# Kernel optimization log

Measured on AMD Instinct MI355X. Metric: run time of the kernel, lower is better.

Reference implementation:

```python
import jax, jax.numpy as jnp
import numpy as np

EMBED_DIMS = 128
NUM_HEADS = 4
NUM_LAYERS = 3
OUT_CHANNELS = 20
PROJECT_SCALE = 4
VOXEL_SIZE = 0.2
SCENE_FULL = (256, 256, 32)
SCENE = tuple(s // PROJECT_SCALE for s in SCENE_FULL)  # (64, 64, 8)
NQ = SCENE[0] * SCENE[1] * SCENE[2]                    # 32768
N_INST = 100
NUM_CLS = 21
IMAGE_SHAPE = (48, 160)
ORI_IMAGE_SHAPE = (384, 1280)
SCORE_THR, MASK_THR, IOU_THR = 0.25, 0.5, 0.8
DILATIONS = (1, 2, 3)


def _generate_grid(grid_shape, value):
    axes = [np.linspace(0, v - 1, s, dtype=np.float32) for s, v in zip(grid_shape, value)]
    return np.stack(np.meshgrid(*axes, indexing='ij'), 0)


def _layer_norm(x, g, b):
    mu = x.mean(-1, keepdims=True)
    var = ((x - mu) ** 2).mean(-1, keepdims=True)
    return (x - mu) * jax.lax.rsqrt(var + 1e-5) * g + b


def _mha(q, k, v, bias, in_w, in_b, out_w, out_b):
    C = q.shape[-1]
    H, D = NUM_HEADS, q.shape[-1] // NUM_HEADS
    wq, wk, wv = jnp.split(in_w, 3, axis=0)
    bq, bk, bv = jnp.split(in_b, 3)
    qh = (q @ wq.T + bq).reshape(q.shape[0], q.shape[1], H, D)
    kh = (k @ wk.T + bk).reshape(k.shape[0], k.shape[1], H, D)
    vh = (v @ wv.T + bv).reshape(v.shape[0], v.shape[1], H, D)
    s = jnp.einsum('bqhd,bkhd->bhqk', qh, kh) * (1.0 / np.sqrt(D)) + bias
    a = jax.nn.softmax(s, axis=-1)
    o = jnp.einsum('bhqk,bkhd->bqhd', a, vh).reshape(q.shape)
    return o @ out_w.T + out_b


def _conv3d(x, w, b, dilation):
    pad = (w.shape[-1] // 2) * dilation
    y = jax.lax.conv_general_dilated(
        x, w, window_strides=(1, 1, 1), padding=[(pad, pad)] * 3,
        rhs_dilation=(dilation,) * 3,
        dimension_numbers=('NCDHW', 'OIDHW', 'NCDHW'))
    return y + b[None, :, None, None, None]


def _forward(inst_queries, pred_logits, pred_masks, depth, K, E, voxel_origin,
             query_embed_w, pos_embed_w, attn_in_w, attn_in_b, attn_out_w,
             attn_out_b, ln1_g, ln1_b, ffn_w1, ffn_b1, ffn_w2, ffn_b2,
             ln2_g, ln2_b, proc_w, proc_b, out_w, out_b, fov_mask):
    C = EMBED_DIMS
    h, w = IMAGE_SHAPE
    n = pred_masks.shape[1]
    # buffers (compile-time constants)
    image_grid = jnp.asarray(_generate_grid(IMAGE_SHAPE, ORI_IMAGE_SHAPE)[::-1].copy())  # [2,h,w] (x,y)
    qp = (_generate_grid(SCENE, SCENE) + 0.5) * VOXEL_SIZE * PROJECT_SCALE
    query_pos0 = jnp.asarray(qp.reshape(3, -1).T)[None]  # [1,NQ,3]

    # panoptic postprocess (masked form, bs=1; invalid instance slots masked, not dropped)
    probs = jax.nn.softmax(jax.nn.sigmoid(pred_logits) / 0.06, axis=-1)
    scores = probs.max(-1)[0]              # [n]; labels.ne(num_classes) always True
    keep0 = scores > SCORE_THR
    pm = jax.nn.sigmoid(pred_masks[0])     # [n,h,w]
    prob_masks = jnp.where(keep0[:, None, None], scores[:, None, None] * pm, -1.0)
    mask_ids = jnp.argmax(prob_masks, axis=0)   # [h,w]
    masks = (mask_ids[None] == jnp.arange(n)[:, None, None]) & keep0[:, None, None]
    mask_area = masks.reshape(n, -1).sum(-1).astype(jnp.float32)
    pm_bin = pm >= MASK_THR
    pm_area = pm_bin.reshape(n, -1).sum(-1).astype(jnp.float32)
    masks = masks & pm_bin
    inter = masks.reshape(n, -1).sum(-1)
    keep = keep0 & (inter > 0) & (mask_area >= IOU_THR * pm_area)
    masks = masks & keep[:, None, None]
    any_keep = keep.any()

    # gather_mask_pos: back-project masked pixels to 3D and sum per instance
    d = depth.reshape(1, 1, h, w)
    grid = jnp.concatenate([image_grid[None] * d, d], axis=1).reshape(1, 3, h * w)
    cam = jnp.linalg.inv(K) @ grid
    hom = jnp.concatenate([cam, jnp.ones((1, 1, h * w), cam.dtype)], axis=1)
    pts = (jnp.linalg.inv(E) @ hom)[0, :3].T       # [HW,3]
    inst_xyz = masks.reshape(n, -1).astype(pts.dtype) @ pts  # [n,3] gather-mask-sum
    inst_pos = (inst_xyz @ pos_embed_w.T)[None]    # [1,n,C]

    # cross-attention over all scene queries; fov gather/scatter folded into final where,
    # valid because per-query computation is independent in cross-attn + per-token FFN/LN.
    qpos = (query_pos0 + voxel_origin) @ pos_embed_w.T        # [1,NQ,C]
    use = jnp.where(any_keep, 1.0, 0.0).astype(inst_queries.dtype)
    kv_k = inst_queries + use * inst_pos
    key_mask = jnp.where(any_keep, keep, True)
    bias = jnp.where(key_mask, 0.0, -1e9)[None, None, None, :]  # [1,1,1,n]
    q = query_embed_w[None]
    for li in range(NUM_LAYERS):
        x = q + qpos
        a = _mha(x, kv_k, inst_queries, bias, attn_in_w[li], attn_in_b[li],
                 attn_out_w[li], attn_out_b[li])
        x = _layer_norm(a + x, ln1_g[li], ln1_b[li])
        f = jax.nn.gelu(x @ ffn_w1[li].T + ffn_b1[li], approximate=False) @ ffn_w2[li].T + ffn_b2[li]
        q = _layer_norm(f + x, ln2_g[li], ln2_b[li])

    q = jnp.where(fov_mask[..., None], q, query_embed_w[None])   # scatter-update query_embed_src[fov_mask]
    x3d = q.reshape(1, *SCENE, C).transpose(0, 4, 1, 2, 3)       # [1,C,X,Y,Z]
    for i, dil in enumerate(DILATIONS):                          # Process: dilated residual convs
        x3d = jax.nn.relu(_conv3d(x3d, proc_w[i], proc_b[i], dil) + x3d)
    return _conv3d(x3d, out_w, out_b, 1)                         # [1,out_ch,X,Y,Z]


def setup_inputs():
    key = jax.random.key(0)
    ks = jax.random.split(key, 16)
    C, L = EMBED_DIMS, NUM_LAYERS
    s = 0.02
    inp = {}
    inp['inst_queries'] = jax.random.normal(ks[0], (1, N_INST, C), jnp.float32)
    inp['pred_logits'] = jax.random.normal(ks[1], (1, N_INST, NUM_CLS), jnp.float32)
    inp['pred_masks'] = jax.random.normal(ks[2], (1, N_INST) + IMAGE_SHAPE, jnp.float32) * 2.0
    inp['depth'] = jax.random.uniform(ks[3], (1,) + IMAGE_SHAPE, jnp.float32, 1.0, 50.0)
    inp['K'] = jnp.array([[[500.0, 0.0, 640.0], [0.0, 500.0, 192.0], [0.0, 0.0, 1.0]]], jnp.float32)
    inp['E'] = jnp.eye(4, dtype=jnp.float32).at[:3, 3].set(jnp.array([0.5, -0.3, 1.2]))[None]
    inp['voxel_origin'] = jax.random.normal(ks[4], (1, 1, 3), jnp.float32)
    inp['query_embed_w'] = jax.random.normal(ks[5], (NQ, C), jnp.float32) * s
    inp['pos_embed_w'] = jax.random.normal(ks[6], (C, 3), jnp.float32) * 2e-4
    inp['attn_in_w'] = jax.random.normal(ks[7], (L, 3 * C, C), jnp.float32) * s
    inp['attn_in_b'] = jnp.zeros((L, 3 * C), jnp.float32)
    inp['attn_out_w'] = jax.random.normal(ks[8], (L, C, C), jnp.float32) * s
    inp['attn_out_b'] = jnp.zeros((L, C), jnp.float32)
    inp['ln1_g'] = jnp.ones((L, C), jnp.float32)
    inp['ln1_b'] = jnp.zeros((L, C), jnp.float32)
    inp['ffn_w1'] = jax.random.normal(ks[9], (L, 4 * C, C), jnp.float32) * s
    inp['ffn_b1'] = jnp.zeros((L, 4 * C), jnp.float32)
    inp['ffn_w2'] = jax.random.normal(ks[10], (L, C, 4 * C), jnp.float32) * s
    inp['ffn_b2'] = jnp.zeros((L, C), jnp.float32)
    inp['ln2_g'] = jnp.ones((L, C), jnp.float32)
    inp['ln2_b'] = jnp.zeros((L, C), jnp.float32)
    inp['proc_w'] = jax.random.normal(ks[11], (3, C, C, 3, 3, 3), jnp.float32) * s
    inp['proc_b'] = jnp.zeros((3, C), jnp.float32)
    inp['out_w'] = jax.random.normal(ks[12], (OUT_CHANNELS, C, 1, 1, 1), jnp.float32) * s
    inp['out_b'] = jnp.zeros((OUT_CHANNELS,), jnp.float32)
    inp['fov_mask'] = jax.random.bernoulli(ks[13], 0.5, (1, NQ))
    return inp


def reference(inst_queries, pred_logits, pred_masks, depth, K, E, voxel_origin,
              query_embed_w, pos_embed_w, attn_in_w, attn_in_b, attn_out_w,
              attn_out_b, ln1_g, ln1_b, ffn_w1, ffn_b1, ffn_w2, ffn_b2,
              ln2_g, ln2_b, proc_w, proc_b, out_w, out_b, fov_mask):
    return _forward(inst_queries, pred_logits, pred_masks, depth, K, E, voxel_origin,
                    query_embed_w, pos_embed_w, attn_in_w, attn_in_b, attn_out_w,
                    attn_out_b, ln1_g, ln1_b, ffn_w1, ffn_b1, ffn_w2, ffn_b2,
                    ln2_g, ln2_b, proc_w, proc_b, out_w, out_b, fov_mask)
```

## Files before the change

kernel.cpp:

```cpp
#include <hip/hip_runtime.h>
#include <math.h>

typedef unsigned short u16;
typedef unsigned int   u32;

#define NQv 32768
#define HWp 7680
#define NI  100

typedef short v8s __attribute__((ext_vector_type(8)));
typedef float v4f __attribute__((ext_vector_type(4)));

__device__ inline float bf2f(u16 u){ u32 x = ((u32)u) << 16; return __uint_as_float(x); }
__device__ inline u16 f2bf(float f){
  u32 x = __float_as_uint(f);
  u32 r = (x + 0x7fffu + ((x >> 16) & 1u)) >> 16;
  return (u16)r;
}
__device__ inline float sigf(float x){ return 1.0f / (1.0f + expf(-x)); }

typedef const __attribute__((address_space(1))) void* gas_t;
typedef __attribute__((address_space(3))) void* las_t;

__global__ void k_prep_small(const float* __restrict__ Km, const float* __restrict__ Em,
                             const float* __restrict__ logits,
                             float* __restrict__ mats, float* __restrict__ scores,
                             int* __restrict__ keep0)
{
  int tid = threadIdx.x;
  if (tid == 0) {
    double a[9];
    for (int i = 0; i < 9; i++) a[i] = (double)Km[i];
    double det = a[0]*(a[4]*a[8]-a[5]*a[7]) - a[1]*(a[3]*a[8]-a[5]*a[6]) + a[2]*(a[3]*a[7]-a[4]*a[6]);
    double id = 1.0 / det;
    double inv[9];
    inv[0]=(a[4]*a[8]-a[5]*a[7])*id; inv[1]=(a[2]*a[7]-a[1]*a[8])*id; inv[2]=(a[1]*a[5]-a[2]*a[4])*id;
    inv[3]=(a[5]*a[6]-a[3]*a[8])*id; inv[4]=(a[0]*a[8]-a[2]*a[6])*id; inv[5]=(a[2]*a[3]-a[0]*a[5])*id;
    inv[6]=(a[3]*a[7]-a[4]*a[6])*id; inv[7]=(a[1]*a[6]-a[0]*a[7])*id; inv[8]=(a[0]*a[4]-a[1]*a[3])*id;
    for (int i = 0; i < 9; i++) mats[i] = (float)inv[i];
    double m[4][8];
    for (int r = 0; r < 4; r++){
      for (int c = 0; c < 4; c++){ m[r][c] = (double)Em[r*4+c]; m[r][4+c] = (r==c) ? 1.0 : 0.0; }
    }
    for (int col = 0; col < 4; col++){
      int piv = col; double best = fabs(m[col][col]);
      for (int r = col+1; r < 4; r++){ double v = fabs(m[r][col]); if (v > best){ best = v; piv = r; } }
      if (piv != col){ for (int c = 0; c < 8; c++){ double t = m[col][c]; m[col][c] = m[piv][c]; m[piv][c] = t; } }
      double p = m[col][col];
      for (int c = 0; c < 8; c++) m[col][c] /= p;
      for (int r = 0; r < 4; r++) if (r != col){ double f = m[r][col]; for (int c = 0; c < 8; c++) m[r][c] -= f*m[col][c]; }
    }
    for (int r = 0; r < 3; r++) for (int c = 0; c < 4; c++) mats[9 + r*4 + c] = (float)m[r][4+c];
  }
  if (tid < NI) {
    float mx = -1e30f;
    for (int c = 0; c < 21; c++){ float t = sigf(logits[tid*21+c]) / 0.06f; mx = fmaxf(mx, t); }
    float s = 0.f;
    for (int c = 0; c < 21; c++){ float t = sigf(logits[tid*21+c]) / 0.06f; s += expf(t - mx); }
    float sc = 1.0f / s;
    scores[tid] = sc;
    keep0[tid] = (sc > 0.25f) ? 1 : 0;
  }
}

__global__ void k_prep_multi(
    const float* __restrict__ s0, u16* __restrict__ d0, int n0,
    const float* __restrict__ s1, u16* __restrict__ d1, int n1,
    const float* __restrict__ s2, u16* __restrict__ d2, int n2,
    const float* __restrict__ s3, u16* __restrict__ d3, int n3,
    u16* __restrict__ z0, int zn0, u16* __restrict__ z1, int zn1,
    u16* __restrict__ z2, int zn2,
    const float* __restrict__ pe, float* __restrict__ peT)
{
  int i = blockIdx.x*256 + threadIdx.x;
  if (i < n0){ d0[i] = f2bf(s0[i]); return; } i -= n0;
  if (i < n1){ d1[i] = f2bf(s1[i]); return; } i -= n1;
  if (i < n2){ d2[i] = f2bf(s2[i]); return; } i -= n2;
  if (i < n3){ d3[i] = f2bf(s3[i]); return; } i -= n3;
  if (i < zn0){ z0[i] = 0; return; } i -= zn0;
  if (i < zn1){ z1[i] = 0; return; } i -= zn1;
  if (i < zn2){ z2[i] = 0; return; } i -= zn2;
  if (i < 384){ int d = i >> 7, c = i & 127; peT[i] = pe[c*3 + d]; }
}

__global__ __launch_bounds__(256) void k_mask_argmax2(
    const float* __restrict__ pmL, const float* __restrict__ scores,
    const int* __restrict__ keep0, int* __restrict__ mids)
{
  __shared__ float sv[4][64];
  __shared__ int   si[4][64];
  int tid = threadIdx.x, lane = tid & 63, w = tid >> 6;
  int p = blockIdx.x*64 + lane;
  float best = -2e30f; int bid = 0;
  #pragma unroll 5
  for (int jj = 0; jj < 25; jj++){
    int i = w*25 + jj;
    float lg = pmL[i*HWp + p];
    float val = keep0[i] ? scores[i] * sigf(lg) : -1.0f;
    if (val > best){ best = val; bid = i; }
  }
  sv[w][lane] = best; si[w][lane] = bid;
  __syncthreads();
  if (w == 0){
    float b0 = sv[0][lane]; int i0 = si[0][lane];
    #pragma unroll
    for (int g = 1; g < 4; g++){
      float bg = sv[g][lane]; int ig = si[g][lane];
      if (bg > b0 || (bg == b0 && ig < i0)){ b0 = bg; i0 = ig; }
    }
    mids[p] = i0;
  }
}

__global__ __launch_bounds__(256) void k_instbp(
    const float* __restrict__ pmL, const int* __restrict__ mids,
    const int* __restrict__ keep0, const float* __restrict__ depth,
    const float* __restrict__ mats, int* __restrict__ keep, float* __restrict__ xyz)
{
  int i = blockIdx.x, tid = threadIdx.x;
  int k0 = keep0[i];
  int ma = 0, pa = 0, it = 0;
  for (int p = tid; p < HWp; p += 256){
    float lg = pmL[i*HWp + p];
    int pb = (lg >= 0.0f) ? 1 : 0;
    int mi = (mids[p] == i && k0) ? 1 : 0;
    ma += mi; pa += pb; it += (mi & pb);
  }
  __shared__ int sma[256], spa[256], sit[256];
  __shared__ int s_keep;
  sma[tid] = ma; spa[tid] = pa; sit[tid] = it;
  __syncthreads();
  for (int off = 128; off; off >>= 1){
    if (tid < off){ sma[tid]+=sma[tid+off]; spa[tid]+=spa[tid+off]; sit[tid]+=sit[tid+off]; }
    __syncthreads();
  }
  if (tid == 0){
    int kk = (k0 && sit[0] > 0 && ((float)sma[0] >= 0.8f*(float)spa[0])) ? 1 : 0;
    keep[i] = kk; s_keep = kk;
  }
  __syncthreads();
  float sx = 0.f, sy = 0.f, sz = 0.f;
  if (s_keep){
    float ik0=mats[0],ik1=mats[1],ik2=mats[2],ik3=mats[3],ik4=mats[4],ik5=mats[5],ik6=mats[6],ik7=mats[7],ik8=mats[8];
    const float* iE = mats + 9;
    for (int p = tid; p < HWp; p += 256){
      if (mids[p] == i && pmL[i*HWp + p] >= 0.0f){
        int r = p / 160, c = p % 160;
        float xg = (float)((double)c * (1279.0/159.0));
        float yg = (float)((double)r * (383.0/47.0));
        float d = depth[p];
        float g0 = xg*d, g1 = yg*d, g2 = d;
        float c0 = ik0*g0 + ik1*g1 + ik2*g2;
        float c1 = ik3*g0 + ik4*g1 + ik5*g2;
        float c2 = ik6*g0 + ik7*g1 + ik8*g2;
        sx += iE[0]*c0 + iE[1]*c1 + iE[2]*c2 + iE[3];
        sy += iE[4]*c0 + iE[5]*c1 + iE[6]*c2 + iE[7];
        sz += iE[8]*c0 + iE[9]*c1 + iE[10]*c2 + iE[11];
      }
    }
  }
  __shared__ float rx[256], ry[256], rz[256];
  rx[tid]=sx; ry[tid]=sy; rz[tid]=sz;
  __syncthreads();
  for (int off = 128; off; off >>= 1){
    if (tid < off){ rx[tid]+=rx[tid+off]; ry[tid]+=ry[tid+off]; rz[tid]+=rz[tid+off]; }
    __syncthreads();
  }
  if (tid == 0){ xyz[i*3+0]=rx[0]; xyz[i*3+1]=ry[0]; xyz[i*3+2]=rz[0]; }
}

__global__ void k_kvk(const float* __restrict__ iq, const float* __restrict__ pe,
                      const float* __restrict__ xyz, const int* __restrict__ keep,
                      float* __restrict__ kvk)
{
  int tid = threadIdx.x;
  unsigned long long b = __ballot(tid < 100 && keep[tid] != 0);
  __shared__ int s_w[4];
  if ((tid & 63) == 0) s_w[tid >> 6] = (b != 0ULL);
  __syncthreads();
  float u = (s_w[0] | s_w[1]) ? 1.0f : 0.0f;
  int idx = blockIdx.x*256 + tid;
  if (idx >= NI*128) return;
  int i = idx >> 7, c = idx & 127;
  float ip = pe[c*3+0]*xyz[i*3+0] + pe[c*3+1]*xyz[i*3+1] + pe[c*3+2]*xyz[i*3+2];
  kvk[idx] = iq[idx] + u * ip;
}

__global__ __launch_bounds__(512) void k_khvh2(const float* __restrict__ kvk,
    const float* __restrict__ iq, const float* __restrict__ Win,
    const float* __restrict__ bin, const int* __restrict__ keep,
    float* __restrict__ biasArr, u16* __restrict__ khs_bf, u16* __restrict__ vt_bf)
{
  __shared__ u16 s_in[NI][130];
  __shared__ u16 s_w[64][130];
  __shared__ int s_any[8];
  int li = blockIdx.x, c0 = blockIdx.y*64;
  bool isK = (c0 < 128);
  const float* srcIn = isK ? kvk : iq;
  int tid = threadIdx.x;
  unsigned long long bm = __ballot(tid < 100 && keep[tid] != 0);
  if ((tid & 63) == 0) s_any[tid >> 6] = (bm != 0ULL);
  for (int i = tid; i < NI*128; i += 512) s_in[i>>7][i&127] = f2bf(srcIn[i]);
  const float* wbase = Win + ((size_t)li*384 + 128 + c0)*128;
  for (int i = tid; i < 64*128; i += 512) s_w[i>>7][i&127] = f2bf(wbase[i]);
  __syncthreads();
  if (li == 0 && c0 == 0 && tid < 128){
    int any = s_any[0] | s_any[1];
    float bb;
    if (tid < NI) bb = any ? (keep[tid] ? 0.0f : -1e9f) : 0.0f;
    else bb = -1e9f;
    biasArr[tid] = bb;
  }
  for (int o = tid; o < NI*64; o += 512){
    int k = o >> 6, c = o & 63;
    float acc = 0.f;
    #pragma unroll 8
    for (int j = 0; j < 128; j++) acc += bf2f(s_in[k][j]) * bf2f(s_w[c][j]);
    int cc = c0 + c;
    float v = acc + bin[li*384 + 128 + cc];
    int ch = cc & 127;
    if (isK) khs_bf[(((size_t)li*4 + (ch>>5))*128 + k)*32 + (ch&31)] = f2bf(v * 0.17677669529663687f);
    else     vt_bf [(((size_t)li*4 + (ch>>5))*32 + (ch&31))*128 + k] = f2bf(v);
  }
}

__global__ __launch_bounds__(256) void k_packconv2(const float* __restrict__ w, u16* __restrict__ wp)
{
  __shared__ u16 s[3456];
  int o = blockIdx.x, li = blockIdx.y;
  const float* src = w + ((size_t)li*128 + o)*3456;
  for (int t = threadIdx.x; t < 3456; t += 256) s[t] = f2bf(src[t]);
  __syncthreads();
  for (int e = threadIdx.x; e < 3456; e += 256){
    int t = e >> 7, i = e & 127;
    wp[(((size_t)li*27 + t)*128 + o)*128 + i] = s[i*27 + t];
  }
}

__device__ inline void stage128(const u16* __restrict__ G, u16* lds,
                                int rbase, int pitchK, int kofs)
{
  int lane = threadIdx.x & 63, w = threadIdx.x >> 6;
  #pragma unroll
  for (int s = 0; s < 4; s++){
    int ldsOff = s*8192 + w*1024 + lane*16;
    int row = ldsOff >> 8;
    int cb  = ldsOff & 255;
    int scb = cb ^ ((row & 7) << 4);
    const u16* src = G + (size_t)(rbase + row)*pitchK + kofs + (scb >> 1);
    u16* dst = lds + (s*4096 + w*512);
    __builtin_amdgcn_global_load_lds((gas_t)src, (las_t)dst, 16, 0, 0);
  }
}

__device__ inline void copy32k(const u16* __restrict__ G, u16* lds)
{
  int lane = threadIdx.x & 63, w = threadIdx.x >> 6;
  #pragma unroll
  for (int s = 0; s < 4; s++){
    int off = s*4096 + w*512;
    const u16* src = G + off + lane*8;
    __builtin_amdgcn_global_load_lds((gas_t)src, (las_t)(lds + off), 16, 0, 0);
  }
}

__device__ inline void stageConvA4(const u16* __restrict__ X, const u16* __restrict__ zp,
                                   u16* lds, int m0, int dx, int dy)
{
  int lane = threadIdx.x & 63, w = threadIdx.x >> 6;
  #pragma unroll
  for (int s = 0; s < 4; s++){
    int ldsOff = s*8192 + w*1024 + lane*16;
    int row = ldsOff >> 8;
    int cb  = ldsOff & 255;
    int scb = cb ^ ((row & 7) << 4);
    int sidx = m0 + row;
    int xs = (sidx >> 9) + dx, ys = ((sidx >> 3) & 63) + dy, zs = sidx & 7;
    bool ok = ((unsigned)xs < 64u) & ((unsigned)ys < 64u);
    const u16* src = ok ? (X + (size_t)((xs*64+ys)*8+zs)*128 + (scb>>1)) : (zp + (scb>>1));
    u16* dst = lds + (s*4096 + w*512);
    __builtin_amdgcn_global_load_lds((gas_t)src, (las_t)dst, 16, 0, 0);
  }
}

__device__ inline v8s fragld(const u16* base, int row, int cb){
  return *(const v8s*)(base + row*128 + (((cb) ^ ((row & 7) << 4)) >> 1));
}

__device__ inline void compute128(const u16* As, const u16* Bs,
                                  int wm, int wn, int r15, int kg, v4f acc[2][4])
{
  #pragma unroll
  for (int k0 = 0; k0 < 4; k0++){
    int cb = k0*64 + kg*16;
    v8s a0 = fragld(As, wm*32 +      r15, cb);
    v8s a1 = fragld(As, wm*32 + 16 + r15, cb);
    v8s b0 = fragld(Bs, wn*64 +      r15, cb);
    v8s b1 = fragld(Bs, wn*64 + 16 + r15, cb);
    v8s b2 = fragld(Bs, wn*64 + 32 + r15, cb);
    v8s b3 = fragld(Bs, wn*64 + 48 + r15, cb);
    acc[0][0] = __builtin_amdgcn_mfma_f32_16x16x32_bf16(a0, b0, acc[0][0], 0, 0, 0);
    acc[0][1] = __builtin_amdgcn_mfma_f32_16x16x32_bf16(a0, b1, acc[0][1], 0, 0, 0);
    acc[0][2] = __builtin_amdgcn_mfma_f32_16x16x32_bf16(a0, b2, acc[0][2], 0, 0, 0);
    acc[0][3] = __builtin_amdgcn_mfma_f32_16x16x32_bf16(a0, b3, acc[0][3], 0, 0, 0);
    acc[1][0] = __builtin_amdgcn_mfma_f32_16x16x32_bf16(a1, b0, acc[1][0], 0, 0, 0);
    acc[1][1] = __builtin_amdgcn_mfma_f32_16x16x32_bf16(a1, b1, acc[1][1], 0, 0, 0);
    acc[1][2] = __builtin_amdgcn_mfma_f32_16x16x32_bf16(a1, b2, acc[1][2], 0, 0, 0);
    acc[1][3] = __builtin_amdgcn_mfma_f32_16x16x32_bf16(a1, b3, acc[1][3], 0, 0, 0);
  }
}

__global__ __launch_bounds__(512) void k_layer(
    const void* __restrict__ srcv, int srcBf,
    const float* __restrict__ peT, const float* __restrict__ vo,
    const u16* __restrict__ ainQ, const float* __restrict__ ainQb,
    const u16* __restrict__ khs, const u16* __restrict__ vt,
    const float* __restrict__ biasArr,
    const u16* __restrict__ aoutw, const float* __restrict__ aoutb,
    const float* __restrict__ g1, const float* __restrict__ b1v,
    const u16* __restrict__ w1p, const float* __restrict__ b1p,
    const u16* __restrict__ w2p, const float* __restrict__ b2p,
    const float* __restrict__ g2, const float* __restrict__ b2v,
    u16* __restrict__ outB, const int* __restrict__ fov, const float* __restrict__ qe)
{
  extern __shared__ u16 smem[];
  u16* SA = smem;
  u16* SB = smem + 16384;
  u16* X  = smem + 32768;
  u16* Rh = smem + 49152;
  char* Xc = (char*)X;
  char* Rc = (char*)Rh;
  int tid = threadIdx.x, lane = tid & 63, w = tid >> 6;
  int wm = w & 3, wn = w >> 2, r15 = lane & 15, kg = lane >> 4;
  int m0 = blockIdx.x * 128;

  stage128(ainQ, SA, 0, 128, 0);
  copy32k(khs, Rh);
  copy32k(vt, Rh + 16384);
  {
    int r = tid >> 2, c0 = (tid & 3)*32;
    int q = m0 + r;
    float px = ((float)(q >> 9)       + 0.5f)*0.8f + vo[0];
    float py = ((float)((q >> 3)&63)  + 0.5f)*0.8f + vo[1];
    float pz = ((float)(q & 7)        + 0.5f)*0.8f + vo[2];
    char* arow = Xc + r*256;
    int rx = (r & 7) << 4;
    if (!srcBf){
      const float4* sp  = (const float4*)((const float*)srcv + (size_t)q*128 + c0);
      const float4* pex = (const float4*)(peT +   0 + c0);
      const float4* pey = (const float4*)(peT + 128 + c0);
      const float4* pez = (const float4*)(peT + 256 + c0);
      #pragma unroll
      for (int j = 0; j < 8; j++){
        float4 v = sp[j];
        float4 ax = pex[j], ay = pey[j], az = pez[j];
        float o0 = v.x + ax.x*px + ay.x*py + az.x*pz;
        float o1 = v.y + ax.y*px + ay.y*py + az.y*pz;
        float o2 = v.z + ax.z*px + ay.z*py + az.z*pz;
        float o3 = v.w + ax.w*px + ay.w*py + az.w*pz;
        int cbyte = (c0 + j*4)*2;
        *(u32*)(arow + ((cbyte    ) ^ rx)) = (u32)f2bf(o0) | ((u32)f2bf(o1) << 16);
        *(u32*)(arow + ((cbyte + 4) ^ rx)) = (u32)f2bf(o2) | ((u32)f2bf(o3) << 16);
      }
    } else {
      const u16* sp = (const u16*)srcv + (size_t)q*128 + c0;
      #pragma unroll
      for (int j = 0; j < 4; j++){
        v8s t = *(const v8s*)(sp + j*8);
        #pragma unroll
        for (int pr = 0; pr < 4; pr++){
          int c = c0 + j*8 + pr*2;
          float e0 = bf2f((u16)t[pr*2])   + peT[c]*px   + peT[128+c]*py   + peT[256+c]*pz;
          float e1 = bf2f((u16)t[pr*2+1]) + peT[c+1]*px + peT[128+c+1]*py + peT[256+c+1]*pz;
          *(u32*)(arow + ((c*2) ^ rx)) = (u32)f2bf(e0) | ((u32)f2bf(e1) << 16);
        }
      }
    }
  }
  __syncthreads();

  {
    v4f acc[2][4] = {};
    compute128(X, SA, wm, wn, r15, kg, acc);
    #pragma unroll
    for (int i = 0; i < 2; i++){
      #pragma unroll
      for (int j = 0; j < 4; j++){
        int col = wn*64 + j*16 + r15;
        float bv = ainQb[col];
        #pragma unroll
        for (int rr = 0; rr < 4; rr++){
          int row = wm*32 + i*16 + kg*4 + rr;
          *(u16*)((char*)SB + row*256 + (((col*2)) ^ ((row & 7) << 4))) = f2bf(acc[i][j][rr] + bv);
        }
      }
    }
  }
  __syncthreads();

  {
    int c = lane & 15, r4 = lane >> 4;
    char* pwc = (char*)(SA + w*2048);
    int qrow_base = w*16;
    #pragma unroll
    for (int h = 0; h < 4; h++){
      const u16* Kh = Rh + h*4096;
      const u16* Vh = Rh + 16384 + h*4096;
      int qrow = qrow_base + c;
      v8s qf = *(const v8s*)((char*)SB + qrow*256 + ((h*64 + r4*16) ^ ((qrow & 7) << 4)));
      v4f s[8] = {{0,0,0,0},{0,0,0,0},{0,0,0,0},{0,0,0,0},{0,0,0,0},{0,0,0,0},{0,0,0,0},{0,0,0,0}};
      #pragma unroll
      for (int kt = 0; kt < 8; kt++){
        v8s kf = *(const v8s*)(Kh + (kt*16 + c)*32 + r4*8);
        s[kt] = __builtin_amdgcn_mfma_f32_16x16x32_bf16(kf, qf, s[kt], 0, 0, 0);
      }
      float mx = -1e30f;
      #pragma unroll
      for (int kt = 0; kt < 8; kt++){
        float4 bb = *(const float4*)(biasArr + kt*16 + r4*4);
        s[kt][0] += bb.x; s[kt][1] += bb.y; s[kt][2] += bb.z; s[kt][3] += bb.w;
        mx = fmaxf(mx, fmaxf(fmaxf(s[kt][0], s[kt][1]), fmaxf(s[kt][2], s[kt][3])));
      }
      mx = fmaxf(mx, __shfl_xor(mx, 16, 64));
      mx = fmaxf(mx, __shfl_xor(mx, 32, 64));
      float sum = 0.f;
      #pragma unroll
      for (int kt = 0; kt < 8; kt++){
        #pragma unroll
        for (int rg = 0; rg < 4; rg++){
          float p = __expf(s[kt][rg] - mx);
          s[kt][rg] = p; sum += p;
        }
      }
      sum += __shfl_xor(sum, 16, 64);
      sum += __shfl_xor(sum, 32, 64);
      float inv = 1.0f / sum;
      int rxq = (c & 7) << 4;
      #pragma unroll
      for (int kt = 0; kt < 8; kt++){
        #pragma unroll
        for (int pr = 0; pr < 2; pr++){
          u32 pk = (u32)f2bf(s[kt][pr*2]*inv) | ((u32)f2bf(s[kt][pr*2+1]*inv) << 16);
          int colb = kt*32 + r4*8 + pr*4;
          *(u32*)(pwc + c*256 + (colb ^ rxq)) = pk;
        }
      }
      v4f o[2] = {{0,0,0,0},{0,0,0,0}};
      #pragma unroll
      for (int ks = 0; ks < 4; ks++){
        v8s aP = *(const v8s*)(pwc + c*256 + ((ks*64 + r4*16) ^ rxq));
        #pragma unroll
        for (int dt = 0; dt < 2; dt++){
          v8s vf = *(const v8s*)(Vh + (dt*16 + c)*128 + ks*32 + r4*8);
          o[dt] = __builtin_amdgcn_mfma_f32_16x16x32_bf16(aP, vf, o[dt], 0, 0, 0);
        }
      }
      #pragma unroll
      for (int dt = 0; dt < 2; dt++){
        #pragma unroll
        for (int rg = 0; rg < 4; rg++){
          int row = qrow_base + r4*4 + rg;
          int col = h*32 + dt*16 + c;
          *(u16*)((char*)SB + row*256 + ((col*2) ^ ((row & 7) << 4))) = f2bf(o[dt][rg]);
        }
      }
    }
  }
  __syncthreads();

  stage128(aoutw, SA, 0, 128, 0);
  __syncthreads();
  {
    v4f acc[2][4] = {};
    compute128(SB, SA, wm, wn, r15, kg, acc);
    #pragma unroll
    for (int i = 0; i < 2; i++){
      #pragma unroll
      for (int j = 0; j < 4; j++){
        int col = wn*64 + j*16 + r15;
        float bv = aoutb[col];
        #pragma unroll
        for (int rr = 0; rr < 4; rr++){
          int row = wm*32 + i*16 + kg*4 + rr;
          float xres = bf2f(*(const u16*)(Xc + row*256 + ((col*2) ^ ((row & 7) << 4))));
          float y = acc[i][j][rr] + bv + xres;
          *(float*)(Rc + row*512 + ((col*4) ^ ((row & 7) << 4))) = y;
        }
      }
    }
  }
  __syncthreads();

  {
    int r = tid >> 2, j4 = tid & 3;
    float vals[32];
    int rx = (r & 7) << 4;
    #pragma unroll
    for (int k = 0; k < 32; k++){
      int c = j4 + 4*k;
      vals[k] = *(const float*)(Rc + r*512 + ((c*4) ^ rx));
    }
    float s = 0.f;
    #pragma unroll
    for (int k = 0; k < 32; k++) s += vals[k];
    s += __shfl_xor(s, 1, 64); s += __shfl_xor(s, 2, 64);
    float mean = s * (1.0f/128.0f);
    float vv = 0.f;
    #pragma unroll
    for (int k = 0; k < 32; k++){ float d = vals[k] - mean; vv += d*d; }
    vv += __shfl_xor(vv, 1, 64); vv += __shfl_xor(vv, 2, 64);
    float rs = rsqrtf(vv*(1.0f/128.0f) + 1e-5f);
    #pragma unroll
    for (int k = 0; k < 32; k++){
      int c = j4 + 4*k;
      float o = (vals[k] - mean)*rs*g1[c] + b1v[c];
      *(float*)(Rc + r*512 + ((c*4) ^ rx)) = o;
      *(u16*)(Xc + r*256 + ((c*2) ^ rx)) = f2bf(o);
    }
  }
  __syncthreads();

  v4f acc2[2][4] = {};
  for (int nt = 0; nt < 4; nt++){
    stage128(w1p, SA, nt*128, 128, 0);
    stage128(w2p, SB, 0, 512, nt*128);
    __syncthreads();
    v4f a1[2][4] = {};
    compute128(X, SA, wm, wn, r15, kg, a1);
    __syncthreads();
    #pragma unroll
    for (int i = 0; i < 2; i++){
      #pragma unroll
      for (int j = 0; j < 4; j++){
        int col = wn*64 + j*16 + r15;
        float bv = b1p[nt*128 + col];
        #pragma unroll
        for (int rr = 0; rr < 4; rr++){
          int row = wm*32 + i*16 + kg*4 + rr;
          float hv = a1[i][j][rr] + bv;
          hv = 0.5f*hv*(1.0f + erff(hv*0.70710678118654752f));
          *(u16*)((char*)SA + row*256 + ((col*2) ^ ((row & 7) << 4))) = f2bf(hv);
        }
      }
    }
    __syncthreads();
    compute128(SA, SB, wm, wn, r15, kg, acc2);
    __syncthreads();
  }

  {
    #pragma unroll
    for (int i = 0; i < 2; i++){
      #pragma unroll
      for (int j = 0; j < 4; j++){
        int col = wn*64 + j*16 + r15;
        float bv = b2p[col];
        #pragma unroll
        for (int rr = 0; rr < 4; rr++){
          int row = wm*32 + i*16 + kg*4 + rr;
          char* p = Rc + row*512 + ((col*4) ^ ((row & 7) << 4));
          float y = acc2[i][j][rr] + bv + *(const float*)p;
          *(float*)p = y;
        }
      }
    }
  }
  __syncthreads();

  {
    int r = tid >> 2, j4 = tid & 3;
    float vals[32];
    int rx = (r & 7) << 4;
    #pragma unroll
    for (int k = 0; k < 32; k++){
      int c = j4 + 4*k;
      vals[k] = *(const float*)(Rc + r*512 + ((c*4) ^ rx));
    }
    float s = 0.f;
    #pragma unroll
    for (int k = 0; k < 32; k++) s += vals[k];
    s += __shfl_xor(s, 1, 64); s += __shfl_xor(s, 2, 64);
    float mean = s * (1.0f/128.0f);
    float vv = 0.f;
    #pragma unroll
    for (int k = 0; k < 32; k++){ float d = vals[k] - mean; vv += d*d; }
    vv += __shfl_xor(vv, 1, 64); vv += __shfl_xor(vv, 2, 64);
    float rs = rsqrtf(vv*(1.0f/128.0f) + 1e-5f);
    int gq = m0 + r;
    #pragma unroll
    for (int k = 0; k < 32; k++){
      int c = j4 + 4*k;
      float o = (vals[k] - mean)*rs*g2[c] + b2v[c];
      if (fov){
        outB[(size_t)gq*128 + c] = f2bf(fov[gq] ? o : qe[(size_t)gq*128 + c]);
      } else {
        outB[(size_t)gq*128 + c] = f2bf(o);
      }
    }
  }
}

__global__ __launch_bounds__(512) void k_conv4(
    const u16* __restrict__ X, const u16* __restrict__ W,
    const float* __restrict__ bias, const u16* __restrict__ zp,
    u16* __restrict__ Y, int dil)
{
  extern __shared__ u16 smem[];
  u16* bufA0 = smem;
  u16* bufA1 = smem + 16384;
  u16* bufW0 = smem + 32768;
  u16* bufW1 = smem + 49152;
  int tid = threadIdx.x, lane = tid & 63, w = tid >> 6;
  int wk = w & 1, wm = (w >> 1) & 1, wn = (w >> 2) & 1;
  int r15 = lane & 15, kg = lane >> 4;
  int bid = blockIdx.x;
  int lb = (bid & 7)*32 + (bid >> 3);
  int m0 = lb*128;
  v4f acc[4][4] = {};
  const v8s vzero = {0,0,0,0,0,0,0,0};
  stageConvA4(X, zp, bufA0, m0, -dil, -dil);
  stage128(W, bufW0, 0, 128, 0);
  for (int g = 0; g < 9; g++){
    const u16* As = (g & 1) ? bufA1 : bufA0;
    #pragma unroll
    for (int dzi = 0; dzi < 3; dzi++){
      int t = g*3 + dzi;
      const u16* Ws = (t & 1) ? bufW1 : bufW0;
      if (t + 1 < 27)
        stage128(W + (size_t)(t+1)*16384, ((t+1)&1) ? bufW1 : bufW0, 0, 128, 0);
      if (dzi == 0 && g < 8){
        int gn = g + 1;
        stageConvA4(X, zp, (gn & 1) ? bufA1 : bufA0, m0, (gn/3 - 1)*dil, (gn%3 - 1)*dil);
      }
      if (dzi == 0){
        if (g < 8) asm volatile("s_waitcnt vmcnt(8)" ::: "memory");
        else       asm volatile("s_waitcnt vmcnt(4)" ::: "memory");
      } else {
        if (t < 26) asm volatile("s_waitcnt vmcnt(4)" ::: "memory");
        else        asm volatile("s_waitcnt vmcnt(0)" ::: "memory");
      }
      __builtin_amdgcn_s_barrier();
      asm volatile("" ::: "memory");
      int zofs = (dzi - 1)*dil;
      bool okz = (unsigned)((r15 & 7) + zofs) < 8u;
      #pragma unroll
      for (int k0 = 0; k0 < 2; k0++){
        int cb = wk*128 + k0*64 + kg*16;
        v8s a[4], b[4];
        #pragma unroll
        for (int q = 0; q < 4; q++){
          int ra = wm*64 + q*16 + r15 + zofs;
          int rc = min(max(ra, 0), 127);
          a[q] = okz ? fragld(As, rc, cb) : vzero;
          b[q] = fragld(Ws, wn*64 + q*16 + r15, cb);
        }
        #pragma unroll
        for (int i = 0; i < 4; i++)
          #pragma unroll
          for (int j = 0; j < 4; j++)
            acc[i][j] = __builtin_amdgcn_mfma_f32_16x16x32_bf16(a[i], b[j], acc[i][j], 0, 0, 0);
      }
      asm volatile("" ::: "memory");
      __builtin_amdgcn_s_barrier();
      asm volatile("" ::: "memory");
    }
  }
  float* red = (float*)smem;
  if (wk == 0){
    #pragma unroll
    for (int i = 0; i < 4; i++)
      #pragma unroll
      for (int j = 0; j < 4; j++)
        #pragma unroll
        for (int rr = 0; rr < 4; rr++)
          red[(wm*64 + i*16 + kg*4 + rr)*128 + wn*64 + j*16 + r15] = acc[i][j][rr];
  }
  __syncthreads();
  if (wk == 1){
    #pragma unroll
    for (int i = 0; i < 4; i++){
      #pragma unroll
      for (int j = 0; j < 4; j++){
        int col = wn*64 + j*16 + r15;
        float bv = bias[col];
        #pragma unroll
        for (int rr = 0; rr < 4; rr++){
          int row = wm*64 + i*16 + kg*4 + rr;
          int grow = m0 + row;
          float v = acc[i][j][rr] + red[row*128 + col] + bv + bf2f(X[(size_t)grow*128 + col]);
          v = fmaxf(v, 0.0f);
          Y[(size_t)grow*128 + col] = f2bf(v);
        }
      }
    }
  }
}

__global__ __launch_bounds__(256) void k_outconv(const u16* __restrict__ X,
    const float* __restrict__ W, const float* __restrict__ B, float* __restrict__ out)
{
  __shared__ float sw[20*128];
  __shared__ float sbb[20];
  int tid = threadIdx.x;
  for (int i = tid; i < 20*128; i += 256) sw[i] = W[i];
  if (tid < 20) sbb[tid] = B[tid];
  __syncthreads();
  int s = blockIdx.x*256 + tid;
  u32 rv[64];
  const u32* xp = (const u32*)(X + (size_t)s*128);
  #pragma unroll
  for (int j = 0; j < 64; j++) rv[j] = xp[j];
  for (int ot = 0; ot < 20; ot++){
    float acc = sbb[ot];
    #pragma unroll
    for (int j = 0; j < 64; j++){
      u32 u = rv[j];
      acc += bf2f((u16)(u & 0xffff))*sw[ot*128 + 2*j] + bf2f((u16)(u >> 16))*sw[ot*128 + 2*j + 1];
    }
    out[(size_t)ot*NQv + s] = acc;
  }
}

extern "C" void kernel_launch(void* const* d_in, const int* in_sizes, int n_in,
                              void* d_out, int out_size, void* d_ws, size_t ws_size,
                              hipStream_t stream)
{
  const float* iq    = (const float*)d_in[0];
  const float* logits= (const float*)d_in[1];
  const float* pmL   = (const float*)d_in[2];
  const float* depth = (const float*)d_in[3];
  const float* Km    = (const float*)d_in[4];
  const float* Em    = (const float*)d_in[5];
  const float* vo    = (const float*)d_in[6];
  const float* qe    = (const float*)d_in[7];
  const float* pe    = (const float*)d_in[8];
  const float* ain_w = (const float*)d_in[9];
  const float* ain_b = (const float*)d_in[10];
  const float* aout_w= (const float*)d_in[11];
  const float* aout_b= (const float*)d_in[12];
  const float* ln1g  = (const float*)d_in[13];
  const float* ln1b  = (const float*)d_in[14];
  const float* w1    = (const float*)d_in[15];
  const float* b1    = (const float*)d_in[16];
  const float* w2    = (const float*)d_in[17];
  const float* b2    = (const float*)d_in[18];
  const float* ln2g  = (const float*)d_in[19];
  const float* ln2b  = (const float*)d_in[20];
  const float* pw    = (const float*)d_in[21];
  const float* pb    = (const float*)d_in[22];
  const float* ow    = (const float*)d_in[23];
  const float* ob    = (const float*)d_in[24];
  const int*   fov   = (const int*)d_in[25];
  float* out = (float*)d_out;

  (void)hipFuncSetAttribute((const void*)k_layer, hipFuncAttributeMaxDynamicSharedMemorySize, 163840);
  (void)hipFuncSetAttribute((const void*)k_conv4, hipFuncAttributeMaxDynamicSharedMemorySize, 131072);

  char* ws = (char*)d_ws;
  size_t off = 0;
  auto alloc = [&](size_t bytes) -> char* {
    char* p = ws + off;
    off = (off + bytes + 255) & ~(size_t)255;
    return p;
  };
  float* mats    = (float*)alloc(32*4);
  float* scores  = (float*)alloc(128*4);
  int*   keep0   = (int*)  alloc(128*4);
  int*   keep    = (int*)  alloc(128*4);
  float* biasArr = (float*)alloc(128*4);
  float* xyz     = (float*)alloc(512*4);
  u16*   zp      = (u16*)  alloc(256);
  float* peT     = (float*)alloc(384*4);
  int*   mids    = (int*)  alloc((size_t)HWp*4);
  float* kvkb    = (float*)alloc((size_t)NI*128*4);
  u16* khs_bf  = (u16*)alloc((size_t)3*4*128*32*2);
  u16* vt_bf   = (u16*)alloc((size_t)3*4*32*128*2);
  u16* ain_bf  = (u16*)alloc((size_t)3*384*128*2);
  u16* aout_bf = (u16*)alloc((size_t)3*128*128*2);
  u16* w1_bf   = (u16*)alloc((size_t)3*512*128*2);
  u16* w2_bf   = (u16*)alloc((size_t)3*128*512*2);
  u16* wc_bf   = (u16*)alloc((size_t)3*27*128*128*2);
  u16* T2bf = (u16*)alloc((size_t)NQv*128*2);
  u16* x3a  = (u16*)alloc((size_t)NQv*128*2);
  u16* x3b  = (u16*)alloc((size_t)NQv*128*2);
  (void)ws_size; (void)in_sizes; (void)n_in; (void)out_size;

  k_prep_small<<<1,128,0,stream>>>(Km, Em, logits, mats, scores, keep0);
  {
    int n0 = 3*384*128, n1 = 3*128*128, n2 = 3*512*128, n3 = 3*128*512;
    int zn0 = 3*4*128*32, zn1 = 3*4*32*128, zn2 = 128;
    int total = n0+n1+n2+n3+zn0+zn1+zn2+384;
    k_prep_multi<<<(total+255)/256,256,0,stream>>>(
        ain_w, ain_bf, n0, aout_w, aout_bf, n1, w1, w1_bf, n2, w2, w2_bf, n3,
        khs_bf, zn0, vt_bf, zn1, zp, zn2, pe, peT);
  }
  k_packconv2<<<dim3(128,3),256,0,stream>>>(pw, wc_bf);
  k_mask_argmax2<<<120,256,0,stream>>>(pmL, scores, keep0, mids);
  k_instbp<<<NI,256,0,stream>>>(pmL, mids, keep0, depth, mats, keep, xyz);
  k_kvk<<<(NI*128+255)/256,256,0,stream>>>(iq, pe, xyz, keep, kvkb);
  { dim3 g(3,4); k_khvh2<<<g,512,0,stream>>>(kvkb, iq, ain_w, ain_b, keep, biasArr, khs_bf, vt_bf); }

  for (int li = 0; li < 3; li++){
    const void* src = (li == 0) ? (const void*)qe : (const void*)T2bf;
    u16* outT = (li < 2) ? T2bf : x3a;
    k_layer<<<256,512,163840,stream>>>(
        src, (li == 0) ? 0 : 1, peT, vo,
        ain_bf + (size_t)li*384*128, ain_b + li*384,
        khs_bf + (size_t)li*16384, vt_bf + (size_t)li*16384, biasArr,
        aout_bf + (size_t)li*128*128, aout_b + li*128,
        ln1g + li*128, ln1b + li*128,
        w1_bf + (size_t)li*512*128, b1 + li*512,
        w2_bf + (size_t)li*128*512, b2 + li*128,
        ln2g + li*128, ln2b + li*128,
        outT, (li == 2) ? fov : nullptr, qe);
  }

  k_conv4<<<256,512,131072,stream>>>(x3a, wc_bf + (size_t)0*27*16384, pb + 0,   zp, x3b, 1);
  k_conv4<<<256,512,131072,stream>>>(x3b, wc_bf + (size_t)1*27*16384, pb + 128, zp, x3a, 2);
  k_conv4<<<256,512,131072,stream>>>(x3a, wc_bf + (size_t)2*27*16384, pb + 256, zp, x3b, 3);
  k_outconv<<<128,256,0,stream>>>(x3b, ow, ob, out);
}
```

Baseline: 361.4 us.

## Double-buffer FFN weight staging and use tanh-approx GELU

Restructures the FFN loop so the next chunk's W1/W2 tiles are staged into a second LDS buffer (reusing the fp32 residual region) while the current chunk computes, removing a barrier-bound serial load phase. The fp32 LayerNorm output is no longer kept in LDS; the second residual is read back from the bf16 copy, which lowers residual precision. The exact erf GELU is replaced with a tanh approximation built on __expf, which is cheaper but numerically slightly different.

```diff
diff --git a/kernel.cpp b/kernel.cpp
--- a/kernel.cpp
+++ b/kernel.cpp
@@ -491,6 +491,8 @@
   }
   __syncthreads();
 
+  stage128(w1p, SA, 0, 128, 0);
+  stage128(w2p, SB, 0, 512, 0);
   {
     int r = tid >> 2, j4 = tid & 3;
     float vals[32];
@@ -514,39 +516,53 @@
     for (int k = 0; k < 32; k++){
       int c = j4 + 4*k;
       float o = (vals[k] - mean)*rs*g1[c] + b1v[c];
-      *(float*)(Rc + r*512 + ((c*4) ^ rx)) = o;
       *(u16*)(Xc + r*256 + ((c*2) ^ rx)) = f2bf(o);
     }
   }
   __syncthreads();
 
   v4f acc2[2][4] = {};
-  for (int nt = 0; nt < 4; nt++){
-    stage128(w1p, SA, nt*128, 128, 0);
-    stage128(w2p, SB, 0, 512, nt*128);
-    __syncthreads();
-    v4f a1[2][4] = {};
-    compute128(X, SA, wm, wn, r15, kg, a1);
-    __syncthreads();
-    #pragma unroll
-    for (int i = 0; i < 2; i++){
-      #pragma unroll
-      for (int j = 0; j < 4; j++){
-        int col = wn*64 + j*16 + r15;
-        float bv = b1p[nt*128 + col];
-        #pragma unroll
-        for (int rr = 0; rr < 4; rr++){
-          int row = wm*32 + i*16 + kg*4 + rr;
-          float hv = a1[i][j][rr] + bv;
-          hv = 0.5f*hv*(1.0f + erff(hv*0.70710678118654752f));
-          *(u16*)((char*)SA + row*256 + ((col*2) ^ ((row & 7) << 4))) = f2bf(hv);
-        }
-      }
-    }
-    __syncthreads();
-    compute128(SA, SB, wm, wn, r15, kg, acc2);
-    __syncthreads();
-  }
+  {
+    u16* pa[2] = {SA, Rh};
+    u16* pb[2] = {SB, Rh + 16384};
+    for (int nt = 0; nt < 4; nt++){
+      u16* Wa = pa[nt & 1];
+      u16* Wb = pb[nt & 1];
+      if (nt > 0) __syncthreads();
+      if (nt < 3){
+        stage128(w1p, pa[(nt+1)&1], (nt+1)*128, 128, 0);
+        stage128(w2p, pb[(nt+1)&1], 0, 512, (nt+1)*128);
+      }
+      v4f a1[2][4] = {};
+      compute128(X, Wa, wm, wn, r15, kg, a1);
+      asm volatile("s_waitcnt lgkmcnt(0)" ::: "memory");
+      __builtin_amdgcn_s_barrier();
+      __builtin_amdgcn_sched_barrier(0);
+      #pragma unroll
+      for (int i = 0; i < 2; i++){
+        #pragma unroll
+        for (int j = 0; j < 4; j++){
+          int col = wn*64 + j*16 + r15;
+          float bv = b1p[nt*128 + col];
+          #pragma unroll
+          for (int rr = 0; rr < 4; rr++){
+            int row = wm*32 + i*16 + kg*4 + rr;
+            float hv = a1[i][j][rr] + bv;
+            float u2 = hv*(0.7978845608028654f + 0.0356774081f*hv*hv);
+            float e = __expf(fmaxf(-2.0f*u2, -60.0f));
+            float th = (1.0f - e)/(1.0f + e);
+            hv = 0.5f*hv*(1.0f + th);
+            *(u16*)((char*)Wa + row*256 + ((col*2) ^ ((row & 7) << 4))) = f2bf(hv);
+          }
+        }
+      }
+      asm volatile("s_waitcnt lgkmcnt(0)" ::: "memory");
+      __builtin_amdgcn_s_barrier();
+      __builtin_amdgcn_sched_barrier(0);
+      compute128(Wa, Wb, wm, wn, r15, kg, acc2);
+    }
+  }
+  __syncthreads();
 
   {
     #pragma unroll
@@ -558,9 +574,9 @@
         #pragma unroll
         for (int rr = 0; rr < 4; rr++){
           int row = wm*32 + i*16 + kg*4 + rr;
-          char* p = Rc + row*512 + ((col*4) ^ ((row & 7) << 4));
-          float y = acc2[i][j][rr] + bv + *(const float*)p;
-          *(float*)p = y;
+          float xres = bf2f(*(const u16*)(Xc + row*256 + ((col*2) ^ ((row & 7) << 4))));
+          float y = acc2[i][j][rr] + bv + xres;
+          *(float*)(Rc + row*512 + ((col*4) ^ ((row & 7) << 4))) = y;
         }
       }
     }
@@ -665,6 +681,7 @@
       asm volatile("" ::: "memory");
     }
   }
+  __syncthreads();
   float* red = (float*)smem;
   if (wk == 0){
     #pragma unroll
```

New measurement: 380.3 us. +5.2%, slower.
